# Kernel optimization log

Measured on AMD Instinct MI355X. Metric: run time of the kernel, lower is better.

## Reference

```python
import jax, jax.numpy as jnp
import numpy as np

T, IN, OUT, GS, L, R = 64, 4096, 12288, 128, 4, 16
G = IN // GS  # 32 groups along in_features


def setup_inputs() -> dict:
    key = jax.random.key(0)
    ks = jax.random.split(key, 7)
    x = jax.random.normal(ks[0], (T, IN), dtype=jnp.float32)
    qweight = jax.random.randint(ks[1], (OUT, IN), 0, 16, dtype=jnp.int32)      # int4 codes 0..15
    zeros = jax.random.randint(ks[2], (OUT, G), 0, 16, dtype=jnp.int32)         # per-group zero points
    scales = jax.random.uniform(ks[3], (OUT, G), dtype=jnp.float32) * 0.02      # per-group scales
    up = jax.random.normal(ks[4], (L, OUT, R), dtype=jnp.float32) * 0.02        # LoRA up weights
    down = jax.random.normal(ks[5], (L, R, IN), dtype=jnp.float32) * 0.02       # LoRA down weights
    lora_scales = jax.random.uniform(ks[6], (L,), dtype=jnp.float32)            # scale*alpha/rank folded
    return dict(x=x, qweight=qweight, zeros=zeros, scales=scales, up=up, down=down, lora_scales=lora_scales)


def _dequant(qweight, zeros, scales):
    # AWQ group dequant: w = (q - zero) * scale, groups of GS along in_features
    q = qweight.reshape(OUT, G, GS).astype(jnp.float32)
    z = zeros.astype(jnp.float32)[:, :, None]
    w = (q - z) * scales[:, :, None]
    return w.reshape(OUT, IN)


def reference(x, qweight, zeros, scales, up, down, lora_scales):
    # base quantized linear: y = x @ dequant(W).T
    w = _dequant(qweight, zeros, scales)
    y = jnp.einsum('ti,oi->to', x, w)
    # all LoRA adapters applied in one batched pass (matches looped accumulate)
    t = jnp.einsum('ti,lri->tlr', x, down)               # [T, L, R]
    y = y + jnp.einsum('tlr,lor,l->to', t, up, lora_scales)
    return y
```

## Files before the change

### kernel.cpp

```cpp
#include <hip/hip_runtime.h>
#include <hip/hip_bf16.h>

#define T_DIM   64
#define IN_DIM  4096
#define OUT_DIM 12288
#define NGROUP  32
#define R_DIM   16
#define LR      64

#define BN 16
#define BK 128
#define NCHUNK (IN_DIM / BK)
#define LDS_STRIDE (BK + 8)

#define KSPLIT 8
#define KSLICE (IN_DIM / KSPLIT)

#define PART_FLOATS (KSPLIT * T_DIM * LR)
#define XBF_BYTE_OFF (PART_FLOATS * 4)

typedef __bf16 bf16x4 __attribute__((ext_vector_type(4)));
typedef __bf16 bf16x8 __attribute__((ext_vector_type(8)));
typedef float  f32x4  __attribute__((ext_vector_type(4)));

__global__ __launch_bounds__(256) void prep_kernel(
    const float* __restrict__ x, const float* __restrict__ down,
    const float* __restrict__ lora_scales, float* __restrict__ part,
    __bf16* __restrict__ xbf)
{
    __shared__ float d_lds[KSLICE];
    const int tid = threadIdx.x;
    const int bid = blockIdx.x;

    if (bid < T_DIM) {
        const float4* xr = (const float4*)(x + bid * IN_DIM);
        __bf16* dst = xbf + bid * IN_DIM;
#pragma unroll
        for (int it = 0; it < 4; ++it) {
            int j = it * 256 + tid;
            float4 v = xr[j];
            bf16x4 b;
            b[0] = (__bf16)v.x; b[1] = (__bf16)v.y;
            b[2] = (__bf16)v.z; b[3] = (__bf16)v.w;
            *(bf16x4*)(dst + j * 4) = b;
        }
        return;
    }

    const int p  = bid - T_DIM;
    const int c  = p & 63;
    const int ks = p >> 6;
    const float* dsl = down + c * IN_DIM + ks * KSLICE;
    for (int j = tid; j < KSLICE / 4; j += 256)
        ((float4*)d_lds)[j] = ((const float4*)dsl)[j];
    __syncthreads();
    const float ls = lora_scales[c >> 4];
    const int wave = tid >> 6, lane = tid & 63;
    for (int t = wave * 2; t < T_DIM; t += 8) {
        const float4* xr0 = (const float4*)(x + t * IN_DIM + ks * KSLICE);
        const float4* xr1 = (const float4*)(x + (t + 1) * IN_DIM + ks * KSLICE);
        float sa = 0.f, sb = 0.f;
#pragma unroll
        for (int j = 0; j < 2; ++j) {
            float4 dv  = ((const float4*)d_lds)[lane + j * 64];
            float4 xa  = xr0[lane + j * 64];
            float4 xb  = xr1[lane + j * 64];
            sa += xa.x * dv.x + xa.y * dv.y + xa.z * dv.z + xa.w * dv.w;
            sb += xb.x * dv.x + xb.y * dv.y + xb.z * dv.z + xb.w * dv.w;
        }
        for (int off = 32; off; off >>= 1) {
            sa += __shfl_down(sa, off);
            sb += __shfl_down(sb, off);
        }
        if (lane == 0) {
            part[(ks * T_DIM + t) * LR + c]     = sa * ls;
            part[(ks * T_DIM + t + 1) * LR + c] = sb * ls;
        }
    }
}

__global__ __launch_bounds__(256) void awq_lora_gemm_kernel(
    const __bf16* __restrict__ xbf, const int* __restrict__ qweight,
    const int* __restrict__ zeros, const float* __restrict__ scales,
    const float* __restrict__ up, const float* __restrict__ part,
    float* __restrict__ out)
{
    __shared__ __bf16 x_lds[2][T_DIM][LDS_STRIDE];
    __shared__ __bf16 w_lds[2][BN][LDS_STRIDE];
    __shared__ float  s_lds[BN][NGROUP];
    __shared__ float  zs_lds[BN][NGROUP];

    const int tid  = threadIdx.x;
    const int n0   = blockIdx.x * BN;
    const int wave = tid >> 6, lane = tid & 63;
    const int lrow = lane & 15, quad = lane >> 4;

    int qrow[2], qcol[2], qoff[2];
#pragma unroll
    for (int it = 0; it < 2; ++it) {
        int e = (it * 256 + tid) * 4;
        qrow[it] = e >> 7; qcol[it] = e & 127;
        qoff[it] = (n0 + qrow[it]) * IN_DIM + qcol[it];
    }
    int xrow[4], xcu[4], xoff[4];
#pragma unroll
    for (int it = 0; it < 4; ++it) {
        int e16 = it * 256 + tid;
        xrow[it] = e16 >> 4; xcu[it] = e16 & 15;
        xoff[it] = xrow[it] * IN_DIM + xcu[it] * 8;
    }

#pragma unroll
    for (int it = 0; it < 2; ++it) {
        int idx = it * 256 + tid;
        int row = idx >> 5, g = idx & 31;
        float s = scales[(n0 + row) * NGROUP + g];
        float z = (float)zeros[(n0 + row) * NGROUP + g];
        s_lds[row][g]  = s;
        zs_lds[row][g] = -z * s;
    }

    int4   qr0[2], qr1[2];
    bf16x8 xr0[4], xr1[4];
#pragma unroll
    for (int it = 0; it < 2; ++it) qr0[it] = *(const int4*)(qweight + qoff[it]);
#pragma unroll
    for (int it = 0; it < 4; ++it) xr0[it] = *(const bf16x8*)(xbf + xoff[it]);
#pragma unroll
    for (int it = 0; it < 2; ++it) qr1[it] = *(const int4*)(qweight + qoff[it] + BK);
#pragma unroll
    for (int it = 0; it < 4; ++it) xr1[it] = *(const bf16x8*)(xbf + xoff[it] + BK);

    f32x4 acc = {0.f, 0.f, 0.f, 0.f};

    __syncthreads();

    for (int ch = 0; ch < NCHUNK; ch += 2) {
#pragma unroll
        for (int it = 0; it < 2; ++it) {
            float s  = s_lds[qrow[it]][ch];
            float zs = zs_lds[qrow[it]][ch];
            bf16x4 w;
            w[0] = (__bf16)((float)qr0[it].x * s + zs);
            w[1] = (__bf16)((float)qr0[it].y * s + zs);
            w[2] = (__bf16)((float)qr0[it].z * s + zs);
            w[3] = (__bf16)((float)qr0[it].w * s + zs);
            *(bf16x4*)&w_lds[0][qrow[it]][qcol[it]] = w;
        }
#pragma unroll
        for (int it = 0; it < 4; ++it)
            *(bf16x8*)&x_lds[0][xrow[it]][xcu[it] * 8] = xr0[it];
        __syncthreads();
        if (ch + 2 < NCHUNK) {
            const int k0 = (ch + 2) * BK;
#pragma unroll
            for (int it = 0; it < 2; ++it) qr0[it] = *(const int4*)(qweight + qoff[it] + k0);
#pragma unroll
            for (int it = 0; it < 4; ++it) xr0[it] = *(const bf16x8*)(xbf + xoff[it] + k0);
        }
#pragma unroll
        for (int kk = 0; kk < 4; ++kk) {
            const int ko = kk * 32 + quad * 8;
            bf16x8 a  = *(const bf16x8*)&x_lds[0][wave * 16 + lrow][ko];
            bf16x8 b0 = *(const bf16x8*)&w_lds[0][lrow][ko];
            acc = __builtin_amdgcn_mfma_f32_16x16x32_bf16(a, b0, acc, 0, 0, 0);
        }

#pragma unroll
        for (int it = 0; it < 2; ++it) {
            float s  = s_lds[qrow[it]][ch + 1];
            float zs = zs_lds[qrow[it]][ch + 1];
            bf16x4 w;
            w[0] = (__bf16)((float)qr1[it].x * s + zs);
            w[1] = (__bf16)((float)qr1[it].y * s + zs);
            w[2] = (__bf16)((float)qr1[it].z * s + zs);
            w[3] = (__bf16)((float)qr1[it].w * s + zs);
            *(bf16x4*)&w_lds[1][qrow[it]][qcol[it]] = w;
        }
#pragma unroll
        for (int it = 0; it < 4; ++it)
            *(bf16x8*)&x_lds[1][xrow[it]][xcu[it] * 8] = xr1[it];
        __syncthreads();
        if (ch + 3 < NCHUNK) {
            const int k0 = (ch + 3) * BK;
#pragma unroll
            for (int it = 0; it < 2; ++it) qr1[it] = *(const int4*)(qweight + qoff[it] + k0);
#pragma unroll
            for (int it = 0; it < 4; ++it) xr1[it] = *(const bf16x8*)(xbf + xoff[it] + k0);
        }
#pragma unroll
        for (int kk = 0; kk < 4; ++kk) {
            const int ko = kk * 32 + quad * 8;
            bf16x8 a  = *(const bf16x8*)&x_lds[1][wave * 16 + lrow][ko];
            bf16x8 b0 = *(const bf16x8*)&w_lds[1][lrow][ko];
            acc = __builtin_amdgcn_mfma_f32_16x16x32_bf16(a, b0, acc, 0, 0, 0);
        }
    }

    {
        const f32x4* p4 = (const f32x4*)part;
#pragma unroll
        for (int it = 0; it < 4; ++it) {
            int u = it * 256 + tid;
            f32x4 s = p4[u];
#pragma unroll
            for (int p = 1; p < KSPLIT; ++p) s += p4[p * 1024 + u];
            bf16x4 bv;
            bv[0] = (__bf16)s[0]; bv[1] = (__bf16)s[1];
            bv[2] = (__bf16)s[2]; bv[3] = (__bf16)s[3];
            *(bf16x4*)&x_lds[0][u >> 4][(u & 15) * 4] = bv;
        }
    }
#pragma unroll
    for (int it = 0; it < 4; ++it) {
        int idx = it * 256 + tid;
        int oo = idx >> 6, cc = idx & 63;
        int l = cc >> 4, r = cc & 15;
        w_lds[0][oo][cc] = (__bf16)up[(l * OUT_DIM + n0 + oo) * R_DIM + r];
    }
    __syncthreads();
#pragma unroll
    for (int kk = 0; kk < 2; ++kk) {
        const int ko = kk * 32 + quad * 8;
        bf16x8 a  = *(const bf16x8*)&x_lds[0][wave * 16 + lrow][ko];
        bf16x8 b0 = *(const bf16x8*)&w_lds[0][lrow][ko];
        acc = __builtin_amdgcn_mfma_f32_16x16x32_bf16(a, b0, acc, 0, 0, 0);
    }

    const int o = n0 + lrow;
#pragma unroll
    for (int i = 0; i < 4; ++i) {
        const int t = wave * 16 + quad * 4 + i;
        out[t * OUT_DIM + o] = acc[i];
    }
}

extern "C" void kernel_launch(void* const* d_in, const int* in_sizes, int n_in,
                              void* d_out, int out_size, void* d_ws, size_t ws_size,
                              hipStream_t stream) {
    const float* x           = (const float*)d_in[0];
    const int*   qweight     = (const int*)d_in[1];
    const int*   zeros       = (const int*)d_in[2];
    const float* scales      = (const float*)d_in[3];
    const float* up          = (const float*)d_in[4];
    const float* down        = (const float*)d_in[5];
    const float* lora_scales = (const float*)d_in[6];
    float*  out  = (float*)d_out;
    float*  part = (float*)d_ws;
    __bf16* xbf  = (__bf16*)((char*)d_ws + XBF_BYTE_OFF);

    hipLaunchKernelGGL(prep_kernel, dim3(T_DIM + 64 * KSPLIT), dim3(256), 0, stream,
                       x, down, lora_scales, part, xbf);
    hipLaunchKernelGGL(awq_lora_gemm_kernel, dim3(OUT_DIM / BN), dim3(256), 0, stream,
                       xbf, qweight, zeros, scales, up, part, out);
}
```

Baseline: 306.5 us.

## Pre-swizzle bf16 activations into MFMA fragment layout and load A directly to registers

The prep kernel now writes the bf16 copy of x in an MFMA-fragment-ordered layout, so each lane in the GEMM kernel loads its A operand straight from global memory into registers. This drops the x tile from LDS, along with its LDS stores and reads, shrinking shared memory per block. Launch bounds now request 4 blocks per CU. Each wave still reads the full activation slice it needs through L2 on every tile, and the tighter launch bound may force the compiler to limit registers.

```diff
diff --git a/kernel.cpp b/kernel.cpp
--- a/kernel.cpp
+++ b/kernel.cpp
@@ -11,7 +11,8 @@
 #define BN 16
 #define BK 128
 #define NCHUNK (IN_DIM / BK)
-#define LDS_STRIDE (BK + 8)
+#define W_STRIDE (BK + 8)
+#define T_STRIDE (LR + 8)
 
 #define KSPLIT 8
 #define KSLICE (IN_DIM / KSPLIT)
@@ -26,28 +27,35 @@
 __global__ __launch_bounds__(256) void prep_kernel(
     const float* __restrict__ x, const float* __restrict__ down,
     const float* __restrict__ lora_scales, float* __restrict__ part,
-    __bf16* __restrict__ xbf)
+    __bf16* __restrict__ xbf2)
 {
-    __shared__ float d_lds[KSLICE];
     const int tid = threadIdx.x;
     const int bid = blockIdx.x;
 
-    if (bid < T_DIM) {
-        const float4* xr = (const float4*)(x + bid * IN_DIM);
-        __bf16* dst = xbf + bid * IN_DIM;
-#pragma unroll
-        for (int it = 0; it < 4; ++it) {
-            int j = it * 256 + tid;
-            float4 v = xr[j];
-            bf16x4 b;
-            b[0] = (__bf16)v.x; b[1] = (__bf16)v.y;
-            b[2] = (__bf16)v.z; b[3] = (__bf16)v.w;
-            *(bf16x4*)(dst + j * 4) = b;
+    if (bid < 64) {
+        const int rt = bid & 3;
+        const int kb_base = (bid >> 2) * 8;
+        const int lane = tid & 63, w = tid >> 6;
+        const int row  = rt * 16 + (lane & 15);
+        const int qd   = lane >> 4;
+#pragma unroll
+        for (int i = 0; i < 2; ++i) {
+            int kb   = kb_base + i * 4 + w;
+            int col0 = kb * 32 + qd * 8;
+            float4 v0 = *(const float4*)(x + row * IN_DIM + col0);
+            float4 v1 = *(const float4*)(x + row * IN_DIM + col0 + 4);
+            bf16x8 b;
+            b[0] = (__bf16)v0.x; b[1] = (__bf16)v0.y;
+            b[2] = (__bf16)v0.z; b[3] = (__bf16)v0.w;
+            b[4] = (__bf16)v1.x; b[5] = (__bf16)v1.y;
+            b[6] = (__bf16)v1.z; b[7] = (__bf16)v1.w;
+            *(bf16x8*)(xbf2 + ((rt * 128 + kb) * 64 + lane) * 8) = b;
         }
         return;
     }
 
-    const int p  = bid - T_DIM;
+    __shared__ float d_lds[KSLICE];
+    const int p  = bid - 64;
     const int c  = p & 63;
     const int ks = p >> 6;
     const float* dsl = down + c * IN_DIM + ks * KSLICE;
@@ -62,9 +70,9 @@
         float sa = 0.f, sb = 0.f;
 #pragma unroll
         for (int j = 0; j < 2; ++j) {
-            float4 dv  = ((const float4*)d_lds)[lane + j * 64];
-            float4 xa  = xr0[lane + j * 64];
-            float4 xb  = xr1[lane + j * 64];
+            float4 dv = ((const float4*)d_lds)[lane + j * 64];
+            float4 xa = xr0[lane + j * 64];
+            float4 xb = xr1[lane + j * 64];
             sa += xa.x * dv.x + xa.y * dv.y + xa.z * dv.z + xa.w * dv.w;
             sb += xb.x * dv.x + xb.y * dv.y + xb.z * dv.z + xb.w * dv.w;
         }
@@ -79,14 +87,14 @@
     }
 }
 
-__global__ __launch_bounds__(256) void awq_lora_gemm_kernel(
-    const __bf16* __restrict__ xbf, const int* __restrict__ qweight,
+__global__ __launch_bounds__(256, 4) void awq_lora_gemm_kernel(
+    const __bf16* __restrict__ xbf2, const int* __restrict__ qweight,
     const int* __restrict__ zeros, const float* __restrict__ scales,
     const float* __restrict__ up, const float* __restrict__ part,
     float* __restrict__ out)
 {
-    __shared__ __bf16 x_lds[2][T_DIM][LDS_STRIDE];
-    __shared__ __bf16 w_lds[2][BN][LDS_STRIDE];
+    __shared__ __bf16 w_lds[2][BN][W_STRIDE];
+    __shared__ __bf16 t_lds[T_DIM][T_STRIDE];
     __shared__ float  s_lds[BN][NGROUP];
     __shared__ float  zs_lds[BN][NGROUP];
 
@@ -102,13 +110,8 @@
         qrow[it] = e >> 7; qcol[it] = e & 127;
         qoff[it] = (n0 + qrow[it]) * IN_DIM + qcol[it];
     }
-    int xrow[4], xcu[4], xoff[4];
-#pragma unroll
-    for (int it = 0; it < 4; ++it) {
-        int e16 = it * 256 + tid;
-        xrow[it] = e16 >> 4; xcu[it] = e16 & 15;
-        xoff[it] = xrow[it] * IN_DIM + xcu[it] * 8;
-    }
+
+    const __bf16* abase = xbf2 + wave * 65536 + lane * 8;
 
 #pragma unroll
     for (int it = 0; it < 2; ++it) {
@@ -121,15 +124,15 @@
     }
 
     int4   qr0[2], qr1[2];
-    bf16x8 xr0[4], xr1[4];
+    bf16x8 ar0[4], ar1[4];
 #pragma unroll
     for (int it = 0; it < 2; ++it) qr0[it] = *(const int4*)(qweight + qoff[it]);
 #pragma unroll
-    for (int it = 0; it < 4; ++it) xr0[it] = *(const bf16x8*)(xbf + xoff[it]);
+    for (int kk = 0; kk < 4; ++kk) ar0[kk] = *(const bf16x8*)(abase + kk * 512);
 #pragma unroll
     for (int it = 0; it < 2; ++it) qr1[it] = *(const int4*)(qweight + qoff[it] + BK);
 #pragma unroll
-    for (int it = 0; it < 4; ++it) xr1[it] = *(const bf16x8*)(xbf + xoff[it] + BK);
+    for (int kk = 0; kk < 4; ++kk) ar1[kk] = *(const bf16x8*)(abase + 2048 + kk * 512);
 
     f32x4 acc = {0.f, 0.f, 0.f, 0.f};
 
@@ -147,23 +150,19 @@
             w[3] = (__bf16)((float)qr0[it].w * s + zs);
             *(bf16x4*)&w_lds[0][qrow[it]][qcol[it]] = w;
         }
-#pragma unroll
-        for (int it = 0; it < 4; ++it)
-            *(bf16x8*)&x_lds[0][xrow[it]][xcu[it] * 8] = xr0[it];
         __syncthreads();
+#pragma unroll
+        for (int kk = 0; kk < 4; ++kk) {
+            const int ko = kk * 32 + quad * 8;
+            bf16x8 b0 = *(const bf16x8*)&w_lds[0][lrow][ko];
+            acc = __builtin_amdgcn_mfma_f32_16x16x32_bf16(ar0[kk], b0, acc, 0, 0, 0);
+        }
         if (ch + 2 < NCHUNK) {
             const int k0 = (ch + 2) * BK;
 #pragma unroll
             for (int it = 0; it < 2; ++it) qr0[it] = *(const int4*)(qweight + qoff[it] + k0);
 #pragma unroll
-            for (int it = 0; it < 4; ++it) xr0[it] = *(const bf16x8*)(xbf + xoff[it] + k0);
-        }
-#pragma unroll
-        for (int kk = 0; kk < 4; ++kk) {
-            const int ko = kk * 32 + quad * 8;
-            bf16x8 a  = *(const bf16x8*)&x_lds[0][wave * 16 + lrow][ko];
-            bf16x8 b0 = *(const bf16x8*)&w_lds[0][lrow][ko];
-            acc = __builtin_amdgcn_mfma_f32_16x16x32_bf16(a, b0, acc, 0, 0, 0);
+            for (int kk = 0; kk < 4; ++kk) ar0[kk] = *(const bf16x8*)(abase + (ch + 2) * 2048 + kk * 512);
         }
 
 #pragma unroll
@@ -177,23 +176,19 @@
             w[3] = (__bf16)((float)qr1[it].w * s + zs);
             *(bf16x4*)&w_lds[1][qrow[it]][qcol[it]] = w;
         }
-#pragma unroll
-        for (int it = 0; it < 4; ++it)
-            *(bf16x8*)&x_lds[1][xrow[it]][xcu[it] * 8] = xr1[it];
         __syncthreads();
+#pragma unroll
+        for (int kk = 0; kk < 4; ++kk) {
+            const int ko = kk * 32 + quad * 8;
+            bf16x8 b0 = *(const bf16x8*)&w_lds[1][lrow][ko];
+            acc = __builtin_amdgcn_mfma_f32_16x16x32_bf16(ar1[kk], b0, acc, 0, 0, 0);
+        }
         if (ch + 3 < NCHUNK) {
             const int k0 = (ch + 3) * BK;
 #pragma unroll
             for (int it = 0; it < 2; ++it) qr1[it] = *(const int4*)(qweight + qoff[it] + k0);
 #pragma unroll
-            for (int it = 0; it < 4; ++it) xr1[it] = *(const bf16x8*)(xbf + xoff[it] + k0);
-        }
-#pragma unroll
-        for (int kk = 0; kk < 4; ++kk) {
-            const int ko = kk * 32 + quad * 8;
-            bf16x8 a  = *(const bf16x8*)&x_lds[1][wave * 16 + lrow][ko];
-            bf16x8 b0 = *(const bf16x8*)&w_lds[1][lrow][ko];
-            acc = __builtin_amdgcn_mfma_f32_16x16x32_bf16(a, b0, acc, 0, 0, 0);
+            for (int kk = 0; kk < 4; ++kk) ar1[kk] = *(const bf16x8*)(abase + (ch + 3) * 2048 + kk * 512);
         }
     }
 
@@ -208,7 +203,7 @@
             bf16x4 bv;
             bv[0] = (__bf16)s[0]; bv[1] = (__bf16)s[1];
             bv[2] = (__bf16)s[2]; bv[3] = (__bf16)s[3];
-            *(bf16x4*)&x_lds[0][u >> 4][(u & 15) * 4] = bv;
+            *(bf16x4*)&t_lds[u >> 4][(u & 15) * 4] = bv;
         }
     }
 #pragma unroll
@@ -222,7 +217,7 @@
 #pragma unroll
     for (int kk = 0; kk < 2; ++kk) {
         const int ko = kk * 32 + quad * 8;
-        bf16x8 a  = *(const bf16x8*)&x_lds[0][wave * 16 + lrow][ko];
+        bf16x8 a  = *(const bf16x8*)&t_lds[wave * 16 + lrow][ko];
         bf16x8 b0 = *(const bf16x8*)&w_lds[0][lrow][ko];
         acc = __builtin_amdgcn_mfma_f32_16x16x32_bf16(a, b0, acc, 0, 0, 0);
     }
@@ -247,10 +242,10 @@
     const float* lora_scales = (const float*)d_in[6];
     float*  out  = (float*)d_out;
     float*  part = (float*)d_ws;
-    __bf16* xbf  = (__bf16*)((char*)d_ws + XBF_BYTE_OFF);
-
-    hipLaunchKernelGGL(prep_kernel, dim3(T_DIM + 64 * KSPLIT), dim3(256), 0, stream,
-                       x, down, lora_scales, part, xbf);
+    __bf16* xbf2 = (__bf16*)((char*)d_ws + XBF_BYTE_OFF);
+
+    hipLaunchKernelGGL(prep_kernel, dim3(64 + 64 * KSPLIT), dim3(256), 0, stream,
+                       x, down, lora_scales, part, xbf2);
     hipLaunchKernelGGL(awq_lora_gemm_kernel, dim3(OUT_DIM / BN), dim3(256), 0, stream,
-                       xbf, qweight, zeros, scales, up, part, out);
+                       xbf2, qweight, zeros, scales, up, part, out);
 }
```

Result: no change. 302.8 us (-1.2%).
